# Optimization experiments

Measured on AMD Instinct MI355X. Metric: run time of the kernel, lower is better.

## Reference

```python
import jax, jax.numpy as jnp
import numpy as np

D_MODEL = 1024
NUM_HEADS = 16
DFF = 4096
LN_EPS = 1e-08
CLIP = 10.0


def setup_inputs() -> dict:
    key = jax.random.key(0)
    ks = jax.random.split(key, 12)
    d, h, f = D_MODEL, NUM_HEADS, DFF
    s = 1.0 / np.sqrt(d)
    inp = {
        "x": jax.random.normal(ks[0], (4, 2048, d), dtype=jnp.float32),
        "wq": jax.random.normal(ks[1], (d, d), dtype=jnp.float32) * s,
        "bq": jnp.zeros((d,), jnp.float32),
        "wk": jax.random.normal(ks[2], (d, d), dtype=jnp.float32) * s,
        "bk": jnp.zeros((d,), jnp.float32),
        "wv": jax.random.normal(ks[3], (d, d), dtype=jnp.float32) * s,
        "bv": jnp.zeros((d,), jnp.float32),
        "wo": jax.random.normal(ks[4], (d, d), dtype=jnp.float32) * s,
        "bo": jnp.zeros((d,), jnp.float32),
        "w1": jax.random.normal(ks[5], (d, f), dtype=jnp.float32) * s,
        "b1": jnp.zeros((f,), jnp.float32),
        "w2": jax.random.normal(ks[6], (f, d), dtype=jnp.float32) * (1.0 / np.sqrt(f)),
        "b2": jnp.zeros((d,), jnp.float32),
        "ln_gamma": jnp.ones((d,), jnp.float32),
        "ln_beta": jnp.zeros((d,), jnp.float32),
    }
    return inp


def layernorm(x, gamma, beta):
    mu = jnp.mean(x, axis=-1, keepdims=True)
    var = jnp.var(x, axis=-1, keepdims=True)
    return (x - mu) * jax.lax.rsqrt(var + LN_EPS) * gamma + beta


def encoder_layer(x, wq, bq, wk, bk, wv, bv, wo, bo, w1, b1, w2, b2, ln_gamma, ln_beta):
    B, S, d = x.shape
    H = NUM_HEADS
    Dh = d // H
    q = (x @ wq + bq).reshape(B, S, H, Dh).transpose(0, 2, 1, 3)  # bhsd
    k = (x @ wk + bk).reshape(B, S, H, Dh).transpose(0, 2, 1, 3)
    v = (x @ wv + bv).reshape(B, S, H, Dh).transpose(0, 2, 1, 3)
    logits = jnp.einsum('bhqd,bhkd->bhqk', q, k) / jnp.sqrt(jnp.float32(Dh))
    logits = jnp.clip(logits, -CLIP, CLIP)
    attn = jax.nn.softmax(logits, axis=-1)
    ctx = jnp.einsum('bhqk,bhkd->bhqd', attn, v)
    ctx = ctx.transpose(0, 2, 1, 3).reshape(B, S, d)
    attn_out = ctx @ wo + bo
    out1 = layernorm(x + attn_out, ln_gamma, ln_beta)
    ffn = jax.nn.relu(out1 @ w1 + b1) @ w2 + b2
    return layernorm(out1 + ffn, ln_gamma, ln_beta)


def reference(x, wq, bq, wk, bk, wv, bv, wo, bo, w1, b1, w2, b2, ln_gamma, ln_beta):
    return encoder_layer(x, wq, bq, wk, bk, wv, bv, wo, bo, w1, b1, w2, b2, ln_gamma, ln_beta)
```

## Files before the change

### kernel.cpp

```cpp
#include <hip/hip_runtime.h>
#include <stdint.h>

#define D_MODEL 1024
#define NHEAD 16
#define DH 64
#define DFF 4096
#define BATCH 4
#define SEQ 2048
#define MTOT (BATCH*SEQ)

#define QSCALE 0.18033688011112043f
#define CLIP2  14.426950408889634f

typedef short short8 __attribute__((ext_vector_type(8)));
typedef float f32x4 __attribute__((ext_vector_type(4)));
typedef unsigned int uint;

__device__ inline unsigned short f2bf(float f) {
  union { float f; unsigned u; } v; v.f = f;
  unsigned r = v.u + 0x7fffu + ((v.u >> 16) & 1u);
  return (unsigned short)(r >> 16);
}
__device__ inline float bf2f(unsigned short b) {
  union { unsigned u; float f; } v; v.u = ((unsigned)b) << 16;
  return v.f;
}
__device__ inline unsigned pack_trunc(float lo, float hi) {
  union { float f; unsigned u; } a, b; a.f = lo; b.f = hi;
  return __builtin_amdgcn_perm(b.u, a.u, 0x07060302u);
}
__device__ __forceinline__ float hw_exp2(float x) {
  return __builtin_amdgcn_exp2f(x);
}
__device__ __forceinline__ void async16(const unsigned short* g, unsigned short* l) {
  __builtin_amdgcn_global_load_lds(
      (const __attribute__((address_space(1))) unsigned int*)g,
      (__attribute__((address_space(3))) unsigned int*)l, 16, 0, 0);
}

__global__ void cast_kernel(const float* __restrict__ in, unsigned short* __restrict__ out, int n4) {
  int i = blockIdx.x * blockDim.x + threadIdx.x;
  if (i < n4) {
    float4 v = ((const float4*)in)[i];
    ushort4 o;
    o.x = f2bf(v.x); o.y = f2bf(v.y); o.z = f2bf(v.z); o.w = f2bf(v.w);
    ((ushort4*)out)[i] = o;
  }
}

__global__ void transpose_weights_kernel(
    const float* __restrict__ wq, const float* __restrict__ wk,
    const float* __restrict__ wv, const float* __restrict__ wo,
    const float* __restrict__ w1, const float* __restrict__ w2,
    unsigned short* __restrict__ wqkvT, unsigned short* __restrict__ woT,
    unsigned short* __restrict__ w1T, unsigned short* __restrict__ w2T) {
  __shared__ __align__(16) unsigned short tile[64][72];
  const int id = blockIdx.x;
  const float* in; unsigned short* out; int K, N, n0, k0; float scale = 1.0f;
  if (id < 1024) {
    const int wi = id >> 8, t = id & 255;
    switch (wi) {
      case 0:  in = wq; out = wqkvT;           scale = QSCALE; break;
      case 1:  in = wk; out = wqkvT + 1048576; break;
      case 2:  in = wv; out = wqkvT + 2097152; break;
      default: in = wo; out = woT;             break;
    }
    K = 1024; N = 1024; n0 = (t & 15) * 64; k0 = (t >> 4) * 64;
  } else if (id < 2048) {
    const int t = id - 1024;
    in = w1; out = w1T; K = 1024; N = 4096; n0 = (t & 63) * 64; k0 = (t >> 6) * 64;
  } else {
    const int t = id - 2048;
    in = w2; out = w2T; K = 4096; N = 1024; n0 = (t & 15) * 64; k0 = (t >> 4) * 64;
  }
  const int tx = threadIdx.x & 15, ty = threadIdx.x >> 4;
#pragma unroll
  for (int j = 0; j < 64; j += 16) {
    float4 v = *(const float4*)(in + (size_t)(k0 + ty + j) * N + n0 + tx * 4);
    tile[tx * 4 + 0][ty + j] = f2bf(v.x * scale);
    tile[tx * 4 + 1][ty + j] = f2bf(v.y * scale);
    tile[tx * 4 + 2][ty + j] = f2bf(v.z * scale);
    tile[tx * 4 + 3][ty + j] = f2bf(v.w * scale);
  }
  __syncthreads();
  const int r = threadIdx.x >> 3, c = threadIdx.x & 7;
#pragma unroll
  for (int j = 0; j < 64; j += 32)
    *(uint4*)(out + (size_t)(n0 + r + j) * K + k0 + c * 8) =
        *(const uint4*)(&tile[r + j][c * 8]);
}

__global__ void bias_concat_kernel(const float* __restrict__ bq, const float* __restrict__ bk,
                                   const float* __restrict__ bv, float* __restrict__ o) {
  int i = blockIdx.x * 256 + threadIdx.x;
  if (i < 3 * D_MODEL) {
    float v = (i < D_MODEL) ? bq[i] * QSCALE
            : (i < 2 * D_MODEL) ? bk[i - D_MODEL] : bv[i - 2 * D_MODEL];
    o[i] = v;
  }
}

__global__ void transpose_v_kernel(const unsigned short* __restrict__ QKV,
                                   unsigned short* __restrict__ Vt) {
  __shared__ unsigned short tile[32][33];
  int bh = blockIdx.z, b = bh >> 4, h = bh & 15;
  int kv0 = blockIdx.x * 32, dh0 = blockIdx.y * 32;
  int tx = threadIdx.x & 31, ty = threadIdx.x >> 5;
#pragma unroll
  for (int j = 0; j < 32; j += 8)
    tile[ty + j][tx] = QKV[(size_t)(b * SEQ + kv0 + ty + j) * 3072 + 2048 + h * DH + dh0 + tx];
  __syncthreads();
#pragma unroll
  for (int j = 0; j < 32; j += 8)
    Vt[(size_t)(bh * DH + dh0 + ty + j) * SEQ + kv0 + tx] = tile[tx][ty + j];
}

#define MFMA_Q(mh, nh)                                                                     \
  _Pragma("unroll")                                                                        \
  for (int ks = 0; ks < 2; ks++) {                                                         \
    _Pragma("unroll")                                                                      \
    for (int i = 0; i < 4; i++) {                                                          \
      _Pragma("unroll")                                                                    \
      for (int nn = 0; nn < 2; nn++) {                                                     \
        acc[(mh)*4 + i][(nh)*2 + nn] = __builtin_amdgcn_mfma_f32_16x16x32_bf16(            \
            af[i][ks], bf[(nh)*2 + nn][ks], acc[(mh)*4 + i][(nh)*2 + nn], 0, 0, 0);        \
      }                                                                                    \
    }                                                                                      \
  }

template<int RELU, int OUT_BF16, int KSPLIT, int BIAS>
__global__ __launch_bounds__(512, 2) void gemm256_bt_kernel(
    const unsigned short* __restrict__ A,
    const unsigned short* __restrict__ Bt,
    const float* __restrict__ bias,
    void* __restrict__ Cout,
    int M, int N, int K) {
  __shared__ __align__(16) unsigned short lds[65536];

  const int nwg = gridDim.x;
  int nid = (blockIdx.x & 7) * (nwg >> 3) + (blockIdx.x >> 3);
  int kh = 0;
  if (KSPLIT == 2) { kh = nid & 1; nid >>= 1; }
  const int GX = N >> 8;
  const int im = nid / GX, in_ = nid % GX;
  const int m0 = im * 256, n0 = in_ * 256;

  const int tid = threadIdx.x;
  const int lane = tid & 63, wave = tid >> 6;
  const int wm = (wave >> 2) * 128, wn = (wave & 3) * 64;
  const int lm = lane & 15, lg = lane >> 4;
  const int rot = lm & 7;
  const int aoff0 = ((lg) ^ rot) << 3;
  const int aoff1 = ((4 + lg) ^ rot) << 3;
  const int arow = (wm + lm) << 6;
  const int brow = (wn + lm) << 6;

  const int kbeg = (KSPLIT == 2) ? kh * (K >> 1) : 0;
  const int nk = ((KSPLIT == 2) ? (K >> 1) : K) >> 6;

  const int rb = tid >> 3;
  const int gcol = (((tid & 7) ^ (rb & 7)) << 3);
  const unsigned short* gA = A  + (size_t)(m0 + rb) * K + kbeg + gcol;
  const unsigned short* gB = Bt + (size_t)(n0 + rb) * K + kbeg + gcol;

  auto stage = [&](const unsigned short* g, int b, int st, unsigned short* seg) {
    async16(g + (size_t)b * 64 * K + (size_t)st * 64, seg + b * 4096 + tid * 8);
  };

  f32x4 acc[8][4] = {};

  {
    unsigned short* A0s = lds;
    unsigned short* B0s = lds + 16384;
    unsigned short* A1s = lds + 32768;
    unsigned short* B1s = lds + 49152;
    stage(gA, 0, 0, A0s); stage(gA, 2, 0, A0s);
    stage(gB, 0, 0, B0s); stage(gB, 1, 0, B0s);
    stage(gA, 1, 0, A0s); stage(gA, 3, 0, A0s);
    stage(gB, 2, 0, B0s); stage(gB, 3, 0, B0s);
    stage(gA, 0, 1, A1s); stage(gA, 2, 1, A1s);
    stage(gB, 0, 1, B1s); stage(gB, 1, 1, B1s);
    stage(gA, 1, 1, A1s); stage(gA, 3, 1, A1s);
    __builtin_amdgcn_s_waitcnt(0x0F76);
    __builtin_amdgcn_s_barrier();
  }

  for (int t = 0; t < nk; ++t) {
    const int cur = t & 1;
    unsigned short* LA = lds + (cur << 15);
    unsigned short* LB = LA + 16384;
    unsigned short* NA = lds + ((cur ^ 1) << 15);
    unsigned short* NB = NA + 16384;
    short8 af[4][2], bf[4][2];

    if (t + 1 < nk) { stage(gB, 2, t + 1, NB); stage(gB, 3, t + 1, NB); }
#pragma unroll
    for (int i = 0; i < 4; i++) {
      af[i][0] = *(const short8*)(LA + arow + i * 1024 + aoff0);
      af[i][1] = *(const short8*)(LA + arow + i * 1024 + aoff1);
    }
#pragma unroll
    for (int n = 0; n < 2; n++) {
      bf[n][0] = *(const short8*)(LB + brow + n * 1024 + aoff0);
      bf[n][1] = *(const short8*)(LB + brow + n * 1024 + aoff1);
    }
    __builtin_amdgcn_s_barrier();
    __builtin_amdgcn_s_setprio(1);
    MFMA_Q(0, 0);
    __builtin_amdgcn_s_setprio(0);
    __builtin_amdgcn_s_barrier();

    if (t + 2 < nk) { stage(gA, 0, t + 2, LA); stage(gA, 2, t + 2, LA); }
#pragma unroll
    for (int n = 2; n < 4; n++) {
      bf[n][0] = *(const short8*)(LB + brow + n * 1024 + aoff0);
      bf[n][1] = *(const short8*)(LB + brow + n * 1024 + aoff1);
    }
    __builtin_amdgcn_s_barrier();
    __builtin_amdgcn_s_setprio(1);
    MFMA_Q(0, 1);
    __builtin_amdgcn_s_setprio(0);
    __builtin_amdgcn_s_barrier();

    if (t + 2 < nk) { stage(gB, 0, t + 2, LB); stage(gB, 1, t + 2, LB); }
#pragma unroll
    for (int i = 0; i < 4; i++) {
      af[i][0] = *(const short8*)(LA + arow + 4096 + i * 1024 + aoff0);
      af[i][1] = *(const short8*)(LA + arow + 4096 + i * 1024 + aoff1);
    }
    __builtin_amdgcn_s_barrier();
    __builtin_amdgcn_s_setprio(1);
    MFMA_Q(1, 1);
    __builtin_amdgcn_s_setprio(0);
    __builtin_amdgcn_s_barrier();

    if (t + 2 < nk) {
      stage(gA, 1, t + 2, LA); stage(gA, 3, t + 2, LA);
      __builtin_amdgcn_s_waitcnt(0x0F76);
    } else {
      __builtin_amdgcn_s_waitcnt(0x0F70);
    }
    __builtin_amdgcn_s_barrier();
    __builtin_amdgcn_s_setprio(1);
    MFMA_Q(1, 0);
    __builtin_amdgcn_s_setprio(0);
    __builtin_amdgcn_s_barrier();
  }

  unsigned short* Cb = (unsigned short*)Cout + (KSPLIT == 2 ? (size_t)kh * M * N : 0);
#pragma unroll
  for (int nt = 0; nt < 4; nt++) {
    int col = n0 + wn + nt * 16 + lm;
    float bv = BIAS ? bias[col] : 0.0f;
#pragma unroll
    for (int mf = 0; mf < 8; mf++) {
#pragma unroll
      for (int r = 0; r < 4; r++) {
        int row = m0 + wm + mf * 16 + lg * 4 + r;
        float v = acc[mf][nt][r] + bv;
        if (RELU) v = fmaxf(v, 0.0f);
        if (OUT_BF16) Cb[(size_t)row * N + col] = f2bf(v);
        else          ((float*)Cout)[(size_t)row * N + col] = v;
      }
    }
  }
}

__global__ __launch_bounds__(256, 4) void attn_kernel(
    const unsigned short* __restrict__ QKV,
    const unsigned short* __restrict__ Vt_g,
    unsigned short* __restrict__ ctx) {
  __shared__ __align__(16) unsigned short Ks[64 * 64];
  __shared__ __align__(16) unsigned short Vs[64 * 64];
  __shared__ __align__(16) unsigned short Ps[4 * 32 * 64];
  const int bh = blockIdx.x, b = bh >> 4, h = bh & 15;
  const int q0 = blockIdx.y * 128;
  const int tid = threadIdx.x, wave = tid >> 6, lane = tid & 63;
  const int lm = lane & 15, lq = lane >> 4;
  const int srow = tid >> 3, scol = (tid & 7) * 8;
  const int rot = (lm & 7) * 8;

  short8 qf[2][2];
#pragma unroll
  for (int ntq = 0; ntq < 2; ntq++) {
    const unsigned short* qp =
        QKV + (size_t)(b * SEQ + q0 + wave * 32 + ntq * 16 + lm) * 3072 + h * DH;
#pragma unroll
    for (int sl = 0; sl < 2; sl++) qf[ntq][sl] = *(const short8*)(qp + sl * 32 + lq * 8);
  }
  const short8 ones = {0x3F80, 0x3F80, 0x3F80, 0x3F80, 0x3F80, 0x3F80, 0x3F80, 0x3F80};
  f32x4 oacc[2][4] = {};
  f32x4 lsum[2] = {};

  const int sdst = srow * 64 + (scol ^ ((srow & 7) * 8));
  const unsigned short* kg = QKV + (size_t)(b * SEQ) * 3072 + D_MODEL + h * DH + scol;
  const unsigned short* vg = Vt_g + (size_t)(bh * DH + srow) * SEQ + scol;

  uint4 kr0 = *(const uint4*)(kg + (size_t)srow * 3072);
  uint4 kr1 = *(const uint4*)(kg + (size_t)(srow + 32) * 3072);
  uint4 vr0 = *(const uint4*)(vg);
  uint4 vr1 = *(const uint4*)(vg + 32 * SEQ);

  for (int it = 0; it < SEQ / 64; it++) {
    *(uint4*)(Ks + sdst)        = kr0;
    *(uint4*)(Ks + sdst + 2048) = kr1;
    *(uint4*)(Vs + sdst)        = vr0;
    *(uint4*)(Vs + sdst + 2048) = vr1;
    __syncthreads();
    if (it + 1 < SEQ / 64) {
      const int kvn = (it + 1) * 64;
      kr0 = *(const uint4*)(kg + (size_t)(kvn + srow) * 3072);
      kr1 = *(const uint4*)(kg + (size_t)(kvn + srow + 32) * 3072);
      vr0 = *(const uint4*)(vg + kvn);
      vr1 = *(const uint4*)(vg + 32 * SEQ + kvn);
    }

#pragma unroll
    for (int mt = 0; mt < 4; mt++) {
      const unsigned short* krow = Ks + (mt * 16 + lm) * 64;
      short8 kf0 = *(const short8*)(krow + ((lq * 8) ^ rot));
      short8 kf1 = *(const short8*)(krow + ((32 + lq * 8) ^ rot));
#pragma unroll
      for (int ntq = 0; ntq < 2; ntq++) {
        f32x4 sa = {0.f, 0.f, 0.f, 0.f};
        sa = __builtin_amdgcn_mfma_f32_16x16x32_bf16(kf0, qf[ntq][0], sa, 0, 0, 0);
        sa = __builtin_amdgcn_mfma_f32_16x16x32_bf16(kf1, qf[ntq][1], sa, 0, 0, 0);
        float p0 = hw_exp2(fminf(sa[0], CLIP2));
        float p1 = hw_exp2(fminf(sa[1], CLIP2));
        float p2 = hw_exp2(fminf(sa[2], CLIP2));
        float p3 = hw_exp2(fminf(sa[3], CLIP2));
        uint2 d;
        d.x = pack_trunc(p0, p1);
        d.y = pack_trunc(p2, p3);
        *(uint2*)(Ps + wave * 2048 + (ntq * 16 + lm) * 64 + ((mt * 16 + lq * 4) ^ rot)) = d;
      }
    }
    __builtin_amdgcn_s_waitcnt(0xC07F);
    short8 pf[2][2];
#pragma unroll
    for (int mq = 0; mq < 2; mq++)
#pragma unroll
      for (int sl = 0; sl < 2; sl++)
        pf[mq][sl] = *(const short8*)(Ps + wave * 2048 + (mq * 16 + lm) * 64 + ((sl * 32 + lq * 8) ^ rot));
#pragma unroll
    for (int nt = 0; nt < 4; nt++) {
      const unsigned short* vrow = Vs + (nt * 16 + lm) * 64;
      short8 vf0 = *(const short8*)(vrow + ((lq * 8) ^ rot));
      short8 vf1 = *(const short8*)(vrow + ((32 + lq * 8) ^ rot));
#pragma unroll
      for (int mq = 0; mq < 2; mq++) {
        oacc[mq][nt] = __builtin_amdgcn_mfma_f32_16x16x32_bf16(pf[mq][0], vf0, oacc[mq][nt], 0, 0, 0);
        oacc[mq][nt] = __builtin_amdgcn_mfma_f32_16x16x32_bf16(pf[mq][1], vf1, oacc[mq][nt], 0, 0, 0);
      }
    }
#pragma unroll
    for (int mq = 0; mq < 2; mq++) {
      lsum[mq] = __builtin_amdgcn_mfma_f32_16x16x32_bf16(pf[mq][0], ones, lsum[mq], 0, 0, 0);
      lsum[mq] = __builtin_amdgcn_mfma_f32_16x16x32_bf16(pf[mq][1], ones, lsum[mq], 0, 0, 0);
    }
    __syncthreads();
  }

#pragma unroll
  for (int mq = 0; mq < 2; mq++) {
    float linv[4];
#pragma unroll
    for (int r = 0; r < 4; r++) linv[r] = 1.0f / lsum[mq][r];
    const size_t rowbase =
        (size_t)(b * SEQ + q0 + wave * 32 + mq * 16 + lq * 4) * D_MODEL + h * DH;
#pragma unroll
    for (int nt = 0; nt < 4; nt++) {
#pragma unroll
      for (int r = 0; r < 4; r++) {
        ctx[rowbase + (size_t)r * D_MODEL + nt * 16 + lm] = f2bf(oacc[mq][nt][r] * linv[r]);
      }
    }
  }
}

template<int B_BF16, int WRITE_BF16, int THREE>
__global__ void ln_kernel(const float* __restrict__ A, const void* __restrict__ Bv,
                          const void* __restrict__ B2v, const float* __restrict__ cbias,
                          const float* __restrict__ gamma, const float* __restrict__ beta,
                          float* __restrict__ outf, unsigned short* __restrict__ outb) {
  const int row = blockIdx.x;
  const int tid = threadIdx.x;
  const size_t base = (size_t)row * D_MODEL + tid * 4;
  float4 xa = *(const float4*)(A + base);
  float4 xb;
  if (B_BF16) {
    ushort4 u = *(const ushort4*)((const unsigned short*)Bv + base);
    xb.x = bf2f(u.x); xb.y = bf2f(u.y); xb.z = bf2f(u.z); xb.w = bf2f(u.w);
  } else {
    xb = *(const float4*)((const float*)Bv + base);
  }
  if (THREE) {
    ushort4 u2 = *(const ushort4*)((const unsigned short*)B2v + base);
    float4 cb = *(const float4*)(cbias + tid * 4);
    xb.x += bf2f(u2.x) + cb.x; xb.y += bf2f(u2.y) + cb.y;
    xb.z += bf2f(u2.z) + cb.z; xb.w += bf2f(u2.w) + cb.w;
  }
  float v0 = xa.x + xb.x, v1 = xa.y + xb.y, v2 = xa.z + xb.z, v3 = xa.w + xb.w;
  float s = v0 + v1 + v2 + v3;
  float sq = v0 * v0 + v1 * v1 + v2 * v2 + v3 * v3;
#pragma unroll
  for (int off = 1; off < 64; off <<= 1) {
    s  += __shfl_xor(s, off);
    sq += __shfl_xor(sq, off);
  }
  __shared__ float red[8];
  int wave = tid >> 6;
  if ((tid & 63) == 0) { red[wave * 2] = s; red[wave * 2 + 1] = sq; }
  __syncthreads();
  s  = red[0] + red[2] + red[4] + red[6];
  sq = red[1] + red[3] + red[5] + red[7];
  float mean = s * (1.0f / D_MODEL);
  float var = sq * (1.0f / D_MODEL) - mean * mean;
  float inv = rsqrtf(var + 1e-8f);
  float4 g  = *(const float4*)(gamma + tid * 4);
  float4 be = *(const float4*)(beta + tid * 4);
  float o0 = (v0 - mean) * inv * g.x + be.x;
  float o1 = (v1 - mean) * inv * g.y + be.y;
  float o2 = (v2 - mean) * inv * g.z + be.z;
  float o3 = (v3 - mean) * inv * g.w + be.w;
  float4 of; of.x = o0; of.y = o1; of.z = o2; of.w = o3;
  *(float4*)(outf + base) = of;
  if (WRITE_BF16) {
    ushort4 ub; ub.x = f2bf(o0); ub.y = f2bf(o1); ub.z = f2bf(o2); ub.w = f2bf(o3);
    *(ushort4*)(outb + base) = ub;
  }
}

extern "C" void kernel_launch(void* const* d_in, const int* in_sizes, int n_in,
                              void* d_out, int out_size, void* d_ws, size_t ws_size,
                              hipStream_t stream) {
  const float* x     = (const float*)d_in[0];
  const float* wq    = (const float*)d_in[1];
  const float* bq    = (const float*)d_in[2];
  const float* wk    = (const float*)d_in[3];
  const float* bk    = (const float*)d_in[4];
  const float* wv    = (const float*)d_in[5];
  const float* bv    = (const float*)d_in[6];
  const float* wo    = (const float*)d_in[7];
  const float* bo    = (const float*)d_in[8];
  const float* w1    = (const float*)d_in[9];
  const float* b1    = (const float*)d_in[10];
  const float* w2    = (const float*)d_in[11];
  const float* b2    = (const float*)d_in[12];
  const float* gamma = (const float*)d_in[13];
  const float* beta  = (const float*)d_in[14];

  char* ws = (char*)d_ws;
  const size_t MB = 1ull << 20;
  unsigned short* xb      = (unsigned short*)(ws + 0 * MB);
  unsigned short* out1b   = (unsigned short*)(ws + 0 * MB);
  unsigned short* ffn2    = (unsigned short*)(ws + 0 * MB);
  unsigned short* wqkvT   = (unsigned short*)(ws + 16 * MB);
  unsigned short* woT     = (unsigned short*)(ws + 22 * MB);
  unsigned short* w1T     = (unsigned short*)(ws + 24 * MB);
  unsigned short* w2T     = (unsigned short*)(ws + 32 * MB);
  float*          bqkv    = (float*)(ws + 40 * MB);
  unsigned short* qkvb    = (unsigned short*)(ws + 41 * MB);
  unsigned short* oprojp  = (unsigned short*)(ws + 41 * MB);
  unsigned short* h1      = (unsigned short*)(ws + 41 * MB);
  unsigned short* Vt_g    = (unsigned short*)(ws + 89 * MB);
  unsigned short* ctx     = (unsigned short*)(ws + 105 * MB);
  float*          out1f   = (float*)(ws + 121 * MB);

  cast_kernel<<<(MTOT * D_MODEL / 4 + 255) / 256, 256, 0, stream>>>(x, xb, MTOT * D_MODEL / 4);
  transpose_weights_kernel<<<3072, 256, 0, stream>>>(
      wq, wk, wv, wo, w1, w2, wqkvT, woT, w1T, w2T);
  bias_concat_kernel<<<12, 256, 0, stream>>>(bq, bk, bv, bqkv);

  gemm256_bt_kernel<0, 1, 1, 1><<<(3072 / 256) * (MTOT / 256), 512, 0, stream>>>(
      xb, wqkvT, bqkv, qkvb, MTOT, 3072, D_MODEL);
  transpose_v_kernel<<<dim3(SEQ / 32, DH / 32, BATCH * NHEAD), 256, 0, stream>>>(qkvb, Vt_g);
  attn_kernel<<<dim3(BATCH * NHEAD, SEQ / 128), 256, 0, stream>>>(qkvb, Vt_g, ctx);

  gemm256_bt_kernel<0, 1, 2, 0><<<2 * (D_MODEL / 256) * (MTOT / 256), 512, 0, stream>>>(
      ctx, woT, nullptr, oprojp, MTOT, D_MODEL, D_MODEL);
  ln_kernel<1, 1, 1><<<MTOT, 256, 0, stream>>>(
      x, oprojp, oprojp + (size_t)MTOT * D_MODEL, bo, gamma, beta, out1f, out1b);
  gemm256_bt_kernel<1, 1, 1, 1><<<(DFF / 256) * (MTOT / 256), 512, 0, stream>>>(
      out1b, w1T, b1, h1, MTOT, DFF, D_MODEL);
  gemm256_bt_kernel<0, 1, 2, 0><<<2 * (D_MODEL / 256) * (MTOT / 256), 512, 0, stream>>>(
      h1, w2T, nullptr, ffn2, MTOT, D_MODEL, DFF);
  ln_kernel<1, 0, 1><<<MTOT, 256, 0, stream>>>(
      out1f, ffn2, ffn2 + (size_t)MTOT * D_MODEL, b2, gamma, beta, (float*)d_out, nullptr);
}
```

Baseline: 530.7 us.

## Fuse preprocessing kernels and write transposed V from QKV GEMM epilogue

```diff
diff --git a/kernel.cpp b/kernel.cpp
--- a/kernel.cpp
+++ b/kernel.cpp
@@ -38,24 +38,33 @@
       (__attribute__((address_space(3))) unsigned int*)l, 16, 0, 0);
 }
 
-__global__ void cast_kernel(const float* __restrict__ in, unsigned short* __restrict__ out, int n4) {
-  int i = blockIdx.x * blockDim.x + threadIdx.x;
-  if (i < n4) {
-    float4 v = ((const float4*)in)[i];
-    ushort4 o;
-    o.x = f2bf(v.x); o.y = f2bf(v.y); o.z = f2bf(v.z); o.w = f2bf(v.w);
-    ((ushort4*)out)[i] = o;
-  }
-}
-
-__global__ void transpose_weights_kernel(
+__global__ void preprocess_kernel(
+    const float* __restrict__ x, unsigned short* __restrict__ xb,
     const float* __restrict__ wq, const float* __restrict__ wk,
     const float* __restrict__ wv, const float* __restrict__ wo,
     const float* __restrict__ w1, const float* __restrict__ w2,
     unsigned short* __restrict__ wqkvT, unsigned short* __restrict__ woT,
-    unsigned short* __restrict__ w1T, unsigned short* __restrict__ w2T) {
+    unsigned short* __restrict__ w1T, unsigned short* __restrict__ w2T,
+    const float* __restrict__ bq, const float* __restrict__ bk,
+    const float* __restrict__ bv_, float* __restrict__ bqkv) {
   __shared__ __align__(16) unsigned short tile[64][72];
-  const int id = blockIdx.x;
+  const int bid = blockIdx.x;
+  if (bid < 8192) {
+    int i = bid * 256 + threadIdx.x;
+    float4 v = ((const float4*)x)[i];
+    ushort4 o;
+    o.x = f2bf(v.x); o.y = f2bf(v.y); o.z = f2bf(v.z); o.w = f2bf(v.w);
+    ((ushort4*)xb)[i] = o;
+    return;
+  }
+  if (bid >= 11264) {
+    int i = (bid - 11264) * 256 + threadIdx.x;
+    float v = (i < D_MODEL) ? bq[i] * QSCALE
+            : (i < 2 * D_MODEL) ? bk[i - D_MODEL] : bv_[i - 2 * D_MODEL];
+    bqkv[i] = v;
+    return;
+  }
+  const int id = bid - 8192;
   const float* in; unsigned short* out; int K, N, n0, k0; float scale = 1.0f;
   if (id < 1024) {
     const int wi = id >> 8, t = id & 255;
@@ -88,31 +97,6 @@
   for (int j = 0; j < 64; j += 32)
     *(uint4*)(out + (size_t)(n0 + r + j) * K + k0 + c * 8) =
         *(const uint4*)(&tile[r + j][c * 8]);
-}
-
-__global__ void bias_concat_kernel(const float* __restrict__ bq, const float* __restrict__ bk,
-                                   const float* __restrict__ bv, float* __restrict__ o) {
-  int i = blockIdx.x * 256 + threadIdx.x;
-  if (i < 3 * D_MODEL) {
-    float v = (i < D_MODEL) ? bq[i] * QSCALE
-            : (i < 2 * D_MODEL) ? bk[i - D_MODEL] : bv[i - 2 * D_MODEL];
-    o[i] = v;
-  }
-}
-
-__global__ void transpose_v_kernel(const unsigned short* __restrict__ QKV,
-                                   unsigned short* __restrict__ Vt) {
-  __shared__ unsigned short tile[32][33];
-  int bh = blockIdx.z, b = bh >> 4, h = bh & 15;
-  int kv0 = blockIdx.x * 32, dh0 = blockIdx.y * 32;
-  int tx = threadIdx.x & 31, ty = threadIdx.x >> 5;
-#pragma unroll
-  for (int j = 0; j < 32; j += 8)
-    tile[ty + j][tx] = QKV[(size_t)(b * SEQ + kv0 + ty + j) * 3072 + 2048 + h * DH + dh0 + tx];
-  __syncthreads();
-#pragma unroll
-  for (int j = 0; j < 32; j += 8)
-    Vt[(size_t)(bh * DH + dh0 + ty + j) * SEQ + kv0 + tx] = tile[tx][ty + j];
 }
 
 #define MFMA_Q(mh, nh)                                                                     \
@@ -128,12 +112,13 @@
     }                                                                                      \
   }
 
-template<int RELU, int OUT_BF16, int KSPLIT, int BIAS>
+template<int RELU, int OUT_BF16, int KSPLIT, int BIAS, int VWRITE>
 __global__ __launch_bounds__(512, 2) void gemm256_bt_kernel(
     const unsigned short* __restrict__ A,
     const unsigned short* __restrict__ Bt,
     const float* __restrict__ bias,
     void* __restrict__ Cout,
+    unsigned short* __restrict__ Vt,
     int M, int N, int K) {
   __shared__ __align__(16) unsigned short lds[65536];
 
@@ -254,19 +239,27 @@
     float bv = BIAS ? bias[col] : 0.0f;
 #pragma unroll
     for (int mf = 0; mf < 8; mf++) {
+      unsigned short u4[4];
 #pragma unroll
       for (int r = 0; r < 4; r++) {
         int row = m0 + wm + mf * 16 + lg * 4 + r;
         float v = acc[mf][nt][r] + bv;
         if (RELU) v = fmaxf(v, 0.0f);
-        if (OUT_BF16) Cb[(size_t)row * N + col] = f2bf(v);
+        if (OUT_BF16) { u4[r] = f2bf(v); Cb[(size_t)row * N + col] = u4[r]; }
         else          ((float*)Cout)[(size_t)row * N + col] = v;
       }
-    }
-  }
-}
-
-__global__ __launch_bounds__(256, 4) void attn_kernel(
+      if (VWRITE && n0 >= 2048) {
+        const int row0 = m0 + wm + mf * 16 + lg * 4;
+        const int d = col - 2048;
+        ushort4 q; q.x = u4[0]; q.y = u4[1]; q.z = u4[2]; q.w = u4[3];
+        *(ushort4*)(Vt + ((size_t)((row0 >> 11) * 16 + (d >> 6)) * 64 + (d & 63)) * SEQ
+                    + (row0 & 2047)) = q;
+      }
+    }
+  }
+}
+
+__global__ __launch_bounds__(256, 5) void attn_kernel(
     const unsigned short* __restrict__ QKV,
     const unsigned short* __restrict__ Vt_g,
     unsigned short* __restrict__ ctx) {
@@ -467,24 +460,21 @@
   unsigned short* ctx     = (unsigned short*)(ws + 105 * MB);
   float*          out1f   = (float*)(ws + 121 * MB);
 
-  cast_kernel<<<(MTOT * D_MODEL / 4 + 255) / 256, 256, 0, stream>>>(x, xb, MTOT * D_MODEL / 4);
-  transpose_weights_kernel<<<3072, 256, 0, stream>>>(
-      wq, wk, wv, wo, w1, w2, wqkvT, woT, w1T, w2T);
-  bias_concat_kernel<<<12, 256, 0, stream>>>(bq, bk, bv, bqkv);
-
-  gemm256_bt_kernel<0, 1, 1, 1><<<(3072 / 256) * (MTOT / 256), 512, 0, stream>>>(
-      xb, wqkvT, bqkv, qkvb, MTOT, 3072, D_MODEL);
-  transpose_v_kernel<<<dim3(SEQ / 32, DH / 32, BATCH * NHEAD), 256, 0, stream>>>(qkvb, Vt_g);
+  preprocess_kernel<<<11276, 256, 0, stream>>>(
+      x, xb, wq, wk, wv, wo, w1, w2, wqkvT, woT, w1T, w2T, bq, bk, bv, bqkv);
+
+  gemm256_bt_kernel<0, 1, 1, 1, 1><<<(3072 / 256) * (MTOT / 256), 512, 0, stream>>>(
+      xb, wqkvT, bqkv, qkvb, Vt_g, MTOT, 3072, D_MODEL);
   attn_kernel<<<dim3(BATCH * NHEAD, SEQ / 128), 256, 0, stream>>>(qkvb, Vt_g, ctx);
 
-  gemm256_bt_kernel<0, 1, 2, 0><<<2 * (D_MODEL / 256) * (MTOT / 256), 512, 0, stream>>>(
-      ctx, woT, nullptr, oprojp, MTOT, D_MODEL, D_MODEL);
+  gemm256_bt_kernel<0, 1, 2, 0, 0><<<2 * (D_MODEL / 256) * (MTOT / 256), 512, 0, stream>>>(
+      ctx, woT, nullptr, oprojp, nullptr, MTOT, D_MODEL, D_MODEL);
   ln_kernel<1, 1, 1><<<MTOT, 256, 0, stream>>>(
       x, oprojp, oprojp + (size_t)MTOT * D_MODEL, bo, gamma, beta, out1f, out1b);
-  gemm256_bt_kernel<1, 1, 1, 1><<<(DFF / 256) * (MTOT / 256), 512, 0, stream>>>(
-      out1b, w1T, b1, h1, MTOT, DFF, D_MODEL);
-  gemm256_bt_kernel<0, 1, 2, 0><<<2 * (D_MODEL / 256) * (MTOT / 256), 512, 0, stream>>>(
-      h1, w2T, nullptr, ffn2, MTOT, D_MODEL, DFF);
+  gemm256_bt_kernel<1, 1, 1, 1, 0><<<(DFF / 256) * (MTOT / 256), 512, 0, stream>>>(
+      out1b, w1T, b1, h1, nullptr, MTOT, DFF, D_MODEL);
+  gemm256_bt_kernel<0, 1, 2, 0, 0><<<2 * (D_MODEL / 256) * (MTOT / 256), 512, 0, stream>>>(
+      h1, w2T, nullptr, ffn2, nullptr, MTOT, D_MODEL, DFF);
   ln_kernel<1, 0, 1><<<MTOT, 256, 0, stream>>>(
       out1f, ffn2, ffn2 + (size_t)MTOT * D_MODEL, b2, gamma, beta, (float*)d_out, nullptr);
 }
```

After: 627.7 us. 1.18x slower.

## Switch GEMM to 32x32x16 MFMA and merge preprocessing kernels into one launch

Applied to the files above, without the earlier changes.

```diff
diff --git a/kernel.cpp b/kernel.cpp
--- a/kernel.cpp
+++ b/kernel.cpp
@@ -14,6 +14,7 @@
 
 typedef short short8 __attribute__((ext_vector_type(8)));
 typedef float f32x4 __attribute__((ext_vector_type(4)));
+typedef float f32x16 __attribute__((ext_vector_type(16)));
 typedef unsigned int uint;
 
 __device__ inline unsigned short f2bf(float f) {
@@ -38,24 +39,33 @@
       (__attribute__((address_space(3))) unsigned int*)l, 16, 0, 0);
 }
 
-__global__ void cast_kernel(const float* __restrict__ in, unsigned short* __restrict__ out, int n4) {
-  int i = blockIdx.x * blockDim.x + threadIdx.x;
-  if (i < n4) {
-    float4 v = ((const float4*)in)[i];
-    ushort4 o;
-    o.x = f2bf(v.x); o.y = f2bf(v.y); o.z = f2bf(v.z); o.w = f2bf(v.w);
-    ((ushort4*)out)[i] = o;
-  }
-}
-
-__global__ void transpose_weights_kernel(
+__global__ void preprocess_kernel(
+    const float* __restrict__ x, unsigned short* __restrict__ xb,
     const float* __restrict__ wq, const float* __restrict__ wk,
     const float* __restrict__ wv, const float* __restrict__ wo,
     const float* __restrict__ w1, const float* __restrict__ w2,
     unsigned short* __restrict__ wqkvT, unsigned short* __restrict__ woT,
-    unsigned short* __restrict__ w1T, unsigned short* __restrict__ w2T) {
+    unsigned short* __restrict__ w1T, unsigned short* __restrict__ w2T,
+    const float* __restrict__ bq, const float* __restrict__ bk,
+    const float* __restrict__ bv_, float* __restrict__ bqkv) {
   __shared__ __align__(16) unsigned short tile[64][72];
-  const int id = blockIdx.x;
+  const int bid = blockIdx.x;
+  if (bid < 8192) {
+    int i = bid * 256 + threadIdx.x;
+    float4 v = ((const float4*)x)[i];
+    ushort4 o;
+    o.x = f2bf(v.x); o.y = f2bf(v.y); o.z = f2bf(v.z); o.w = f2bf(v.w);
+    ((ushort4*)xb)[i] = o;
+    return;
+  }
+  if (bid >= 11264) {
+    int i = (bid - 11264) * 256 + threadIdx.x;
+    float v = (i < D_MODEL) ? bq[i] * QSCALE
+            : (i < 2 * D_MODEL) ? bk[i - D_MODEL] : bv_[i - 2 * D_MODEL];
+    bqkv[i] = v;
+    return;
+  }
+  const int id = bid - 8192;
   const float* in; unsigned short* out; int K, N, n0, k0; float scale = 1.0f;
   if (id < 1024) {
     const int wi = id >> 8, t = id & 255;
@@ -90,16 +100,6 @@
         *(const uint4*)(&tile[r + j][c * 8]);
 }
 
-__global__ void bias_concat_kernel(const float* __restrict__ bq, const float* __restrict__ bk,
-                                   const float* __restrict__ bv, float* __restrict__ o) {
-  int i = blockIdx.x * 256 + threadIdx.x;
-  if (i < 3 * D_MODEL) {
-    float v = (i < D_MODEL) ? bq[i] * QSCALE
-            : (i < 2 * D_MODEL) ? bk[i - D_MODEL] : bv[i - 2 * D_MODEL];
-    o[i] = v;
-  }
-}
-
 __global__ void transpose_v_kernel(const unsigned short* __restrict__ QKV,
                                    unsigned short* __restrict__ Vt) {
   __shared__ unsigned short tile[32][33];
@@ -115,16 +115,13 @@
     Vt[(size_t)(bh * DH + dh0 + ty + j) * SEQ + kv0 + tx] = tile[tx][ty + j];
 }
 
-#define MFMA_Q(mh, nh)                                                                     \
+#define MFMA_Q32(mh, nh)                                                                   \
   _Pragma("unroll")                                                                        \
-  for (int ks = 0; ks < 2; ks++) {                                                         \
+  for (int ks = 0; ks < 4; ks++) {                                                         \
     _Pragma("unroll")                                                                      \
-    for (int i = 0; i < 4; i++) {                                                          \
-      _Pragma("unroll")                                                                    \
-      for (int nn = 0; nn < 2; nn++) {                                                     \
-        acc[(mh)*4 + i][(nh)*2 + nn] = __builtin_amdgcn_mfma_f32_16x16x32_bf16(            \
-            af[i][ks], bf[(nh)*2 + nn][ks], acc[(mh)*4 + i][(nh)*2 + nn], 0, 0, 0);        \
-      }                                                                                    \
+    for (int i = 0; i < 2; i++) {                                                          \
+      acc[(mh)*2 + i][(nh)] = __builtin_amdgcn_mfma_f32_32x32x16_bf16(                     \
+          af[i][ks], bf[(nh)][ks], acc[(mh)*2 + i][(nh)], 0, 0, 0);                        \
     }                                                                                      \
   }
 
@@ -148,12 +145,13 @@
   const int tid = threadIdx.x;
   const int lane = tid & 63, wave = tid >> 6;
   const int wm = (wave >> 2) * 128, wn = (wave & 3) * 64;
-  const int lm = lane & 15, lg = lane >> 4;
-  const int rot = lm & 7;
-  const int aoff0 = ((lg) ^ rot) << 3;
-  const int aoff1 = ((4 + lg) ^ rot) << 3;
-  const int arow = (wm + lm) << 6;
-  const int brow = (wn + lm) << 6;
+  const int l31 = lane & 31, lh = lane >> 5;
+  const int rot = lane & 7;
+  int aoff[4];
+#pragma unroll
+  for (int ks = 0; ks < 4; ks++) aoff[ks] = (((ks * 2 + lh) ^ rot) << 3);
+  const int arow = (wm + l31) << 6;
+  const int brow = (wn + l31) << 6;
 
   const int kbeg = (KSPLIT == 2) ? kh * (K >> 1) : 0;
   const int nk = ((KSPLIT == 2) ? (K >> 1) : K) >> 6;
@@ -167,7 +165,7 @@
     async16(g + (size_t)b * 64 * K + (size_t)st * 64, seg + b * 4096 + tid * 8);
   };
 
-  f32x4 acc[8][4] = {};
+  f32x16 acc[4][2] = {};
 
   {
     unsigned short* A0s = lds;
@@ -191,46 +189,42 @@
     unsigned short* LB = LA + 16384;
     unsigned short* NA = lds + ((cur ^ 1) << 15);
     unsigned short* NB = NA + 16384;
-    short8 af[4][2], bf[4][2];
+    short8 af[2][4], bf[2][4];
 
     if (t + 1 < nk) { stage(gB, 2, t + 1, NB); stage(gB, 3, t + 1, NB); }
 #pragma unroll
-    for (int i = 0; i < 4; i++) {
-      af[i][0] = *(const short8*)(LA + arow + i * 1024 + aoff0);
-      af[i][1] = *(const short8*)(LA + arow + i * 1024 + aoff1);
-    }
-#pragma unroll
-    for (int n = 0; n < 2; n++) {
-      bf[n][0] = *(const short8*)(LB + brow + n * 1024 + aoff0);
-      bf[n][1] = *(const short8*)(LB + brow + n * 1024 + aoff1);
-    }
+    for (int i = 0; i < 2; i++)
+#pragma unroll
+      for (int ks = 0; ks < 4; ks++)
+        af[i][ks] = *(const short8*)(LA + arow + i * 2048 + aoff[ks]);
+#pragma unroll
+    for (int ks = 0; ks < 4; ks++)
+      bf[0][ks] = *(const short8*)(LB + brow + aoff[ks]);
     __builtin_amdgcn_s_barrier();
     __builtin_amdgcn_s_setprio(1);
-    MFMA_Q(0, 0);
+    MFMA_Q32(0, 0);
     __builtin_amdgcn_s_setprio(0);
     __builtin_amdgcn_s_barrier();
 
     if (t + 2 < nk) { stage(gA, 0, t + 2, LA); stage(gA, 2, t + 2, LA); }
 #pragma unroll
-    for (int n = 2; n < 4; n++) {
-      bf[n][0] = *(const short8*)(LB + brow + n * 1024 + aoff0);
-      bf[n][1] = *(const short8*)(LB + brow + n * 1024 + aoff1);
-    }
+    for (int ks = 0; ks < 4; ks++)
+      bf[1][ks] = *(const short8*)(LB + brow + 2048 + aoff[ks]);
     __builtin_amdgcn_s_barrier();
     __builtin_amdgcn_s_setprio(1);
-    MFMA_Q(0, 1);
+    MFMA_Q32(0, 1);
     __builtin_amdgcn_s_setprio(0);
     __builtin_amdgcn_s_barrier();
 
     if (t + 2 < nk) { stage(gB, 0, t + 2, LB); stage(gB, 1, t + 2, LB); }
 #pragma unroll
-    for (int i = 0; i < 4; i++) {
-      af[i][0] = *(const short8*)(LA + arow + 4096 + i * 1024 + aoff0);
-      af[i][1] = *(const short8*)(LA + arow + 4096 + i * 1024 + aoff1);
-    }
+    for (int i = 0; i < 2; i++)
+#pragma unroll
+      for (int ks = 0; ks < 4; ks++)
+        af[i][ks] = *(const short8*)(LA + arow + (i + 2) * 2048 + aoff[ks]);
     __builtin_amdgcn_s_barrier();
     __builtin_amdgcn_s_setprio(1);
-    MFMA_Q(1, 1);
+    MFMA_Q32(1, 1);
     __builtin_amdgcn_s_setprio(0);
     __builtin_amdgcn_s_barrier();
 
@@ -242,25 +236,29 @@
     }
     __builtin_amdgcn_s_barrier();
     __builtin_amdgcn_s_setprio(1);
-    MFMA_Q(1, 0);
+    MFMA_Q32(1, 0);
     __builtin_amdgcn_s_setprio(0);
     __builtin_amdgcn_s_barrier();
   }
 
   unsigned short* Cb = (unsigned short*)Cout + (KSPLIT == 2 ? (size_t)kh * M * N : 0);
 #pragma unroll
-  for (int nt = 0; nt < 4; nt++) {
-    int col = n0 + wn + nt * 16 + lm;
-    float bv = BIAS ? bias[col] : 0.0f;
-#pragma unroll
-    for (int mf = 0; mf < 8; mf++) {
-#pragma unroll
-      for (int r = 0; r < 4; r++) {
-        int row = m0 + wm + mf * 16 + lg * 4 + r;
-        float v = acc[mf][nt][r] + bv;
-        if (RELU) v = fmaxf(v, 0.0f);
-        if (OUT_BF16) Cb[(size_t)row * N + col] = f2bf(v);
-        else          ((float*)Cout)[(size_t)row * N + col] = v;
+  for (int j = 0; j < 2; j++) {
+    const int col = n0 + wn + j * 32 + l31;
+    const float bvv = BIAS ? bias[col] : 0.0f;
+#pragma unroll
+    for (int ig = 0; ig < 4; ig++) {
+      const int rowbase = m0 + wm + ig * 32 + 4 * lh;
+#pragma unroll
+      for (int g = 0; g < 4; g++) {
+#pragma unroll
+        for (int q = 0; q < 4; q++) {
+          const int row = rowbase + 8 * g + q;
+          float v = acc[ig][j][g * 4 + q] + bvv;
+          if (RELU) v = fmaxf(v, 0.0f);
+          if (OUT_BF16) Cb[(size_t)row * N + col] = f2bf(v);
+          else          ((float*)Cout)[(size_t)row * N + col] = v;
+        }
       }
     }
   }
@@ -467,10 +465,8 @@
   unsigned short* ctx     = (unsigned short*)(ws + 105 * MB);
   float*          out1f   = (float*)(ws + 121 * MB);
 
-  cast_kernel<<<(MTOT * D_MODEL / 4 + 255) / 256, 256, 0, stream>>>(x, xb, MTOT * D_MODEL / 4);
-  transpose_weights_kernel<<<3072, 256, 0, stream>>>(
-      wq, wk, wv, wo, w1, w2, wqkvT, woT, w1T, w2T);
-  bias_concat_kernel<<<12, 256, 0, stream>>>(bq, bk, bv, bqkv);
+  preprocess_kernel<<<11276, 256, 0, stream>>>(
+      x, xb, wq, wk, wv, wo, w1, w2, wqkvT, woT, w1T, w2T, bq, bk, bv, bqkv);
 
   gemm256_bt_kernel<0, 1, 1, 1><<<(3072 / 256) * (MTOT / 256), 512, 0, stream>>>(
       xb, wqkvT, bqkv, qkvb, MTOT, 3072, D_MODEL);
```

Result: no change. 532.8 us (+0.4%).
